# Performance work log

Measured on AMD Instinct MI355X. Metric: run time of the kernel, lower is better.

## Reference

```python
import jax, jax.numpy as jnp
import numpy as np

B, C, H, W = 4, 256, 64, 64
CK = C // 8   # 32, theta/phi channels
CV = C // 2   # 128, g channels


def setup_inputs() -> dict:
    key = jax.random.key(0)
    ks = jax.random.split(key, 10)
    s = lambda fan: 1.0 / np.sqrt(fan)
    inp = {
        "x": jax.random.normal(ks[0], (B, C, H, W), dtype=jnp.float32),
        "theta_w": jax.random.normal(ks[1], (CK, C), dtype=jnp.float32) * s(C),
        "theta_b": jax.random.normal(ks[2], (CK,), dtype=jnp.float32) * 0.01,
        "phi_w": jax.random.normal(ks[3], (CK, C), dtype=jnp.float32) * s(C),
        "phi_b": jax.random.normal(ks[4], (CK,), dtype=jnp.float32) * 0.01,
        "g_w": jax.random.normal(ks[5], (CV, C), dtype=jnp.float32) * s(C),
        "g_b": jax.random.normal(ks[6], (CV,), dtype=jnp.float32) * 0.01,
        "o_w": jax.random.normal(ks[7], (C, CV), dtype=jnp.float32) * s(CV),
        "o_b": jax.random.normal(ks[8], (C,), dtype=jnp.float32) * 0.01,
        "gamma": jax.random.normal(ks[9], (1,), dtype=jnp.float32) * 0.1,
    }
    return inp


def reference(x, theta_w, theta_b, phi_w, phi_b, g_w, g_b, o_w, o_b, gamma):
    b, c, h, w = x.shape
    n = h * w
    xf = x.reshape(b, c, n)  # [B, C, N]
    # 1x1 convs == per-pixel linear projections
    theta = jnp.einsum('oc,bcn->bon', theta_w, xf) + theta_b[None, :, None]  # [B, CK, N]
    phi = jnp.einsum('oc,bcn->bon', phi_w, xf) + phi_b[None, :, None]        # [B, CK, N]
    g = jnp.einsum('oc,bcn->bon', g_w, xf) + g_b[None, :, None]              # [B, CV, N]
    # scores[b, i, j] = theta_i . phi_j ; softmax over dim=1 (query axis i) as in torch code
    scores = jnp.einsum('bci,bcj->bij', theta, phi)  # [B, N, N]
    attention = jax.nn.softmax(scores, axis=1)
    # o_pre = bmm(g, attention^T): o_pre[b, c, i] = sum_j g[b, c, j] * attention[b, i, j]
    o_pre = jnp.einsum('bcj,bij->bci', g, attention)  # [B, CV, N]
    o = jnp.einsum('oc,bcn->bon', o_w, o_pre) + o_b[None, :, None]  # [B, C, N]
    out = (gamma[0] * o + xf).reshape(b, c, h, w)
    return out
```

## Files before the change

kernel.cpp:

```cpp
#include <hip/hip_runtime.h>
#include <math.h>

#define B_  4
#define C_  256
#define N_  4096
#define CK_ 32
#define CV_ 128

typedef __attribute__((ext_vector_type(8))) short short8;
typedef __attribute__((ext_vector_type(4))) float f32x4;
typedef unsigned short u16;
typedef unsigned int   u32;

static constexpr float LOG2E = 1.4426950408889634f;

static __device__ __forceinline__ u16 f2bf(float f) {
    u32 u = __float_as_uint(f);
    u = (u + 0x7FFFu + ((u >> 16) & 1u)) >> 16;
    return (u16)u;
}
static __device__ __forceinline__ float bf2f(u16 h) {
    return __uint_as_float(((u32)h) << 16);
}

__global__ __launch_bounds__(256) void wconv_kernel(
    const float* __restrict__ theta_w, const float* __restrict__ phi_w,
    const float* __restrict__ g_w,     const float* __restrict__ o_w,
    u16* __restrict__ W16, u16* __restrict__ ow16)
{
    const int idx = blockIdx.x * 256 + threadIdx.x;
    if (idx < 8192)        W16[idx] = f2bf(theta_w[idx] * LOG2E);
    else if (idx < 16384)  W16[idx] = f2bf(phi_w[idx - 8192]);
    else if (idx < 49152)  W16[idx] = f2bf(g_w[idx - 16384]);
    else                   ow16[idx - 49152] = f2bf(o_w[idx - 49152]);
}

__global__ __launch_bounds__(256) void xt_kernel(
    const float* __restrict__ x, u16* __restrict__ xT16)
{
    const int b = blockIdx.z, c0 = blockIdx.y * 64, n0 = blockIdx.x * 64;
    const int t = threadIdx.x;
    __shared__ float tile[64][65];

    const int cr = t >> 4, nc = (t & 15) * 4;
    #pragma unroll
    for (int it = 0; it < 4; ++it) {
        const float4 v = *(const float4*)(x + (size_t)(b * C_ + c0 + cr + it * 16) * N_ + n0 + nc);
        tile[cr + it * 16][nc + 0] = v.x; tile[cr + it * 16][nc + 1] = v.y;
        tile[cr + it * 16][nc + 2] = v.z; tile[cr + it * 16][nc + 3] = v.w;
    }
    __syncthreads();
    const int n = t >> 2, cg = (t & 3) * 16;
    union { u16 us[16]; uint4 u4[2]; } pk;
    #pragma unroll
    for (int e = 0; e < 16; ++e) pk.us[e] = f2bf(tile[cg + e][n]);
    uint4* dst = (uint4*)(xT16 + (size_t)(b * N_ + n0 + n) * C_ + c0 + cg);
    dst[0] = pk.u4[0]; dst[1] = pk.u4[1];
}

__global__ __launch_bounds__(256) void proj_mfma_kernel(
    const u16* __restrict__ xT16, const u16* __restrict__ W16,
    const float* __restrict__ theta_b, const float* __restrict__ phi_b,
    const float* __restrict__ g_b,
    u16* __restrict__ theta_t, u16* __restrict__ phi_t, u16* __restrict__ g16)
{
    const int b = blockIdx.y, n0 = blockIdx.x * 64;
    const int w = threadIdx.x >> 6, lane = threadIdx.x & 63;
    const int lr = lane & 15, q = lane >> 4;
    const f32x4 zf = {0.f, 0.f, 0.f, 0.f};

    const u16* xrow = xT16 + (size_t)(b * N_ + n0 + w * 16 + lr) * C_;
    f32x4 acc[4];
    #pragma unroll
    for (int nt = 0; nt < 4; ++nt) acc[nt] = zf;
    for (int ks = 0; ks < 8; ++ks) {
        const short8 aX = *(const short8*)(xrow + ks * 32 + q * 8);
        #pragma unroll
        for (int nt = 0; nt < 4; ++nt) {
            const short8 bW = *(const short8*)(W16 + (size_t)(nt * 16 + lr) * C_ + ks * 32 + q * 8);
            acc[nt] = __builtin_amdgcn_mfma_f32_16x16x32_bf16(aX, bW, acc[nt], 0, 0, 0);
        }
    }
    #pragma unroll
    for (int nt = 0; nt < 4; ++nt) {
        const int o = nt * 16 + lr;
        #pragma unroll
        for (int reg = 0; reg < 4; ++reg) {
            const int n = n0 + w * 16 + q * 4 + reg;
            if (nt < 2)
                theta_t[(size_t)(b * N_ + n) * CK_ + o] = f2bf(acc[nt][reg] + theta_b[o] * LOG2E);
            else
                phi_t[(size_t)(b * N_ + n) * CK_ + (o - 32)] = f2bf(acc[nt][reg] + phi_b[o - 32]);
        }
    }

    #pragma unroll
    for (int mp = 0; mp < 2; ++mp) {
        const int crow = (w * 2 + mp) * 16;
        f32x4 ag[4];
        #pragma unroll
        for (int nt = 0; nt < 4; ++nt) ag[nt] = zf;
        for (int ks = 0; ks < 8; ++ks) {
            const short8 aW = *(const short8*)(W16 + (size_t)(64 + crow + lr) * C_ + ks * 32 + q * 8);
            #pragma unroll
            for (int nt = 0; nt < 4; ++nt) {
                const short8 bX = *(const short8*)(xT16 + (size_t)(b * N_ + n0 + nt * 16 + lr) * C_ + ks * 32 + q * 8);
                ag[nt] = __builtin_amdgcn_mfma_f32_16x16x32_bf16(aW, bX, ag[nt], 0, 0, 0);
            }
        }
        #pragma unroll
        for (int nt = 0; nt < 4; ++nt) {
            #pragma unroll
            for (int reg = 0; reg < 4; ++reg) {
                const int c = crow + q * 4 + reg;
                const int n = n0 + nt * 16 + lr;
                g16[(size_t)(b * CV_ + c) * N_ + n] = f2bf(ag[nt][reg] + g_b[c]);
            }
        }
    }
}

__global__ __launch_bounds__(256) void colstats_kernel(
    const u16* __restrict__ theta_t, const u16* __restrict__ phi_t,
    float* __restrict__ Z)
{
    const int b  = blockIdx.z;
    const int j0 = blockIdx.x * 32;
    const int istart = blockIdx.y * (N_ / 4);
    const int tid = threadIdx.x;
    const int wave = tid >> 6, lane = tid & 63;
    const int lr = lane & 15, q = lane >> 4;

    const int jW = j0 + (wave & 1) * 16;
    const short8 bF = *(const short8*)(phi_t + (size_t)(b * N_ + jW + lr) * CK_ + q * 8);

    const u16* thp = theta_t + (size_t)b * N_ * CK_;
    const f32x4 zero = {0.f, 0.f, 0.f, 0.f};
    float zacc = 0.f;
    for (int it = istart + (wave >> 1) * 16; it < istart + N_ / 4; it += 32) {
        const short8 aF = *(const short8*)(thp + (size_t)(it + lr) * CK_ + q * 8);
        f32x4 S = __builtin_amdgcn_mfma_f32_16x16x32_bf16(aF, bF, zero, 0, 0, 0);
        zacc += exp2f(S[0]) + exp2f(S[1]) + exp2f(S[2]) + exp2f(S[3]);
    }
    zacc += __shfl_xor(zacc, 16);
    zacc += __shfl_xor(zacc, 32);
    if (lane < 16) atomicAdd(&Z[(size_t)b * N_ + jW + lr], zacc);
}

__global__ __launch_bounds__(256) void gscale_kernel(
    u16* __restrict__ g16, const float* __restrict__ Z)
{
    const size_t idx = ((size_t)blockIdx.x * 256 + threadIdx.x) * 8;
    const int n = (int)(idx & (N_ - 1));
    const int b = (int)(idx / ((size_t)CV_ * N_));
    uint4 raw = *(const uint4*)(g16 + idx);
    const float4 z0 = *(const float4*)(Z + (size_t)b * N_ + n);
    const float4 z1 = *(const float4*)(Z + (size_t)b * N_ + n + 4);
    const float zz[8] = {z0.x, z0.y, z0.z, z0.w, z1.x, z1.y, z1.z, z1.w};
    u16* pr = (u16*)&raw;
    union { u16 us[8]; uint4 u4; } pk;
    #pragma unroll
    for (int k = 0; k < 8; ++k) pk.us[k] = f2bf(bf2f(pr[k]) / zz[k]);
    *(uint4*)(g16 + idx) = pk.u4;
}

__global__ __launch_bounds__(512, 4) void opre_kernel(
    const u16* __restrict__ theta_t, const u16* __restrict__ phi_t,
    const u16* __restrict__ g16, float* __restrict__ o_p0, float* __restrict__ o_p1)
{
    const int b = blockIdx.z, jh = blockIdx.y, i0 = blockIdx.x * 64;
    const int w = threadIdx.x >> 6, lane = threadIdx.x & 63;
    const int lr = lane & 15, q = lane >> 4;

    __shared__ u16 El[2][64 * 64];
    __shared__ float rp[16 * 132];

    const int jt = w & 3, it2 = w >> 2;
    const short8 aF0 = *(const short8*)(theta_t + (size_t)(b * N_ + i0 + it2 * 32 + lr) * CK_ + q * 8);
    const short8 aF1 = *(const short8*)(theta_t + (size_t)(b * N_ + i0 + it2 * 32 + 16 + lr) * CK_ + q * 8);

    const int cw = w * 16;
    const u16* gb = g16 + (size_t)(b * CV_ + cw + lr) * N_;
    const u16* pb = phi_t + (size_t)(b * N_) * CK_;

    const f32x4 zf = {0.f, 0.f, 0.f, 0.f};
    f32x4 acc[4];
    #pragma unroll
    for (int nt = 0; nt < 4; ++nt) acc[nt] = zf;

    const int jstart = jh * (N_ / 2), jend = jstart + N_ / 2;
    short8 bF = *(const short8*)(pb + (size_t)(jstart + jt * 16 + lr) * CK_ + q * 8);
    int buf = 0;

    for (int j0 = jstart; j0 < jend; j0 += 64) {
        const short8 gA0 = *(const short8*)(gb + j0 + q * 8);
        const short8 gA1 = *(const short8*)(gb + j0 + 32 + q * 8);

        const f32x4 S0 = __builtin_amdgcn_mfma_f32_16x16x32_bf16(aF0, bF, zf, 0, 0, 0);
        const f32x4 S1 = __builtin_amdgcn_mfma_f32_16x16x32_bf16(aF1, bF, zf, 0, 0, 0);

        const int jn = (j0 + 64 < jend) ? j0 + 64 : jstart;
        bF = *(const short8*)(pb + (size_t)(jn + jt * 16 + lr) * CK_ + q * 8);

        u16* Eb = El[buf];
        const int jcol = jt * 16 + lr;
        #pragma unroll
        for (int reg = 0; reg < 4; ++reg) {
            const int ia = it2 * 32 + q * 4 + reg;
            Eb[ia * 64 + ((((jcol >> 3) ^ (ia & 7)) << 3) | (jcol & 7))] = f2bf(exp2f(S0[reg]));
            const int ib = ia + 16;
            Eb[ib * 64 + ((((jcol >> 3) ^ (ib & 7)) << 3) | (jcol & 7))] = f2bf(exp2f(S1[reg]));
        }
        __syncthreads();

        #pragma unroll
        for (int nt = 0; nt < 4; ++nt) {
            const int row = nt * 16 + lr;
            const short8 bE0 = *(const short8*)(Eb + row * 64 + ((q ^ (row & 7)) << 3));
            const short8 bE1 = *(const short8*)(Eb + row * 64 + (((4 + q) ^ (row & 7)) << 3));
            acc[nt] = __builtin_amdgcn_mfma_f32_16x16x32_bf16(gA0, bE0, acc[nt], 0, 0, 0);
            acc[nt] = __builtin_amdgcn_mfma_f32_16x16x32_bf16(gA1, bE1, acc[nt], 0, 0, 0);
        }
        buf ^= 1;
    }

    __syncthreads();
    float* op = (jh ? o_p1 : o_p0) + (size_t)(b * N_ + i0) * CV_;
    #pragma unroll
    for (int p = 0; p < 4; ++p) {
        #pragma unroll
        for (int reg = 0; reg < 4; ++reg)
            rp[lr * 132 + cw + q * 4 + reg] = acc[p][reg];
        __syncthreads();
        const int t = threadIdx.x;
        const int ir = t >> 5, cc = (t & 31) * 4;
        *(float4*)(op + (size_t)(p * 16 + ir) * CV_ + cc) = *(const float4*)(rp + ir * 132 + cc);
        __syncthreads();
    }
}

__global__ __launch_bounds__(256) void final_mfma_kernel(
    const float* __restrict__ o_p0, const float* __restrict__ o_p1,
    const u16* __restrict__ ow16, const float* __restrict__ o_b,
    const float* __restrict__ gamma, const float* __restrict__ x,
    float* __restrict__ out)
{
    const int b = blockIdx.y, n0 = blockIdx.x * 64;
    const int w = threadIdx.x >> 6, lane = threadIdx.x & 63;
    const int lr = lane & 15, q = lane >> 4;
    const f32x4 zf = {0.f, 0.f, 0.f, 0.f};

    f32x4 acc[4][4];
    #pragma unroll
    for (int mt = 0; mt < 4; ++mt)
        #pragma unroll
        for (int nt = 0; nt < 4; ++nt) acc[mt][nt] = zf;

    const float* p0 = o_p0 + (size_t)(b * N_ + n0) * CV_;
    const float* p1 = o_p1 + (size_t)(b * N_ + n0) * CV_;

    for (int ks = 0; ks < 4; ++ks) {
        short8 bP[4];
        #pragma unroll
        for (int nt = 0; nt < 4; ++nt) {
            const size_t base = (size_t)(nt * 16 + lr) * CV_ + ks * 32 + q * 8;
            const float4 a0 = *(const float4*)(p0 + base);
            const float4 a1 = *(const float4*)(p0 + base + 4);
            const float4 b0 = *(const float4*)(p1 + base);
            const float4 b1 = *(const float4*)(p1 + base + 4);
            union { u16 us[8]; short8 s8; } pk;
            pk.us[0] = f2bf(a0.x + b0.x); pk.us[1] = f2bf(a0.y + b0.y);
            pk.us[2] = f2bf(a0.z + b0.z); pk.us[3] = f2bf(a0.w + b0.w);
            pk.us[4] = f2bf(a1.x + b1.x); pk.us[5] = f2bf(a1.y + b1.y);
            pk.us[6] = f2bf(a1.z + b1.z); pk.us[7] = f2bf(a1.w + b1.w);
            bP[nt] = pk.s8;
        }
        #pragma unroll
        for (int mt = 0; mt < 4; ++mt) {
            const short8 aW = *(const short8*)(ow16 + (size_t)((w * 4 + mt) * 16 + lr) * CV_ + ks * 32 + q * 8);
            #pragma unroll
            for (int nt = 0; nt < 4; ++nt)
                acc[mt][nt] = __builtin_amdgcn_mfma_f32_16x16x32_bf16(aW, bP[nt], acc[mt][nt], 0, 0, 0);
        }
    }

    const float gm = gamma[0];
    #pragma unroll
    for (int mt = 0; mt < 4; ++mt) {
        #pragma unroll
        for (int nt = 0; nt < 4; ++nt) {
            #pragma unroll
            for (int reg = 0; reg < 4; ++reg) {
                const int oc = (w * 4 + mt) * 16 + q * 4 + reg;
                const int n = n0 + nt * 16 + lr;
                const size_t off = (size_t)(b * C_ + oc) * N_ + n;
                out[off] = x[off] + gm * (acc[mt][nt][reg] + o_b[oc]);
            }
        }
    }
}

extern "C" void kernel_launch(void* const* d_in, const int* in_sizes, int n_in,
                              void* d_out, int out_size, void* d_ws, size_t ws_size,
                              hipStream_t stream)
{
    const float* x       = (const float*)d_in[0];
    const float* theta_w = (const float*)d_in[1];
    const float* theta_b = (const float*)d_in[2];
    const float* phi_w   = (const float*)d_in[3];
    const float* phi_b   = (const float*)d_in[4];
    const float* g_w     = (const float*)d_in[5];
    const float* g_b     = (const float*)d_in[6];
    const float* o_w     = (const float*)d_in[7];
    const float* o_b     = (const float*)d_in[8];
    const float* gamma   = (const float*)d_in[9];
    float* out = (float*)d_out;

    u16* xT16    = (u16*)d_ws;
    u16* W16     = xT16 + (size_t)B_ * N_ * C_;
    u16* ow16    = W16 + 192 * C_;
    u16* theta_t = ow16 + C_ * CV_;
    u16* phi_t   = theta_t + (size_t)B_ * N_ * CK_;
    u16* g16     = phi_t + (size_t)B_ * N_ * CK_;
    float* Z     = (float*)(g16 + (size_t)B_ * CV_ * N_);
    float* o_p0  = Z + (size_t)B_ * N_;
    float* o_p1  = o_p0 + (size_t)B_ * N_ * CV_;

    hipMemsetAsync(Z, 0, (size_t)B_ * N_ * sizeof(float), stream);

    wconv_kernel<<<dim3(320), 256, 0, stream>>>(theta_w, phi_w, g_w, o_w, W16, ow16);
    xt_kernel<<<dim3(N_ / 64, C_ / 64, B_), 256, 0, stream>>>(x, xT16);
    proj_mfma_kernel<<<dim3(N_ / 64, B_), 256, 0, stream>>>(
        xT16, W16, theta_b, phi_b, g_b, theta_t, phi_t, g16);
    colstats_kernel<<<dim3(N_ / 32, 4, B_), 256, 0, stream>>>(theta_t, phi_t, Z);
    gscale_kernel<<<dim3((B_ * CV_ * N_) / 2048), 256, 0, stream>>>(g16, Z);
    opre_kernel<<<dim3(N_ / 64, 2, B_), 512, 0, stream>>>(theta_t, phi_t, g16, o_p0, o_p1);
    final_mfma_kernel<<<dim3(N_ / 64, B_), 256, 0, stream>>>(
        o_p0, o_p1, ow16, o_b, gamma, x, out);
}
```

Baseline: 205.4 us.

## Fold softmax normalization into opre, keep E in registers, bf16 partials

Drops the gscale pass and applies the reciprocal column sums inside opre. opre now computes S transposed (phi as A, theta as B), so the exp results already sit in the MFMA A-operand layout for the 16x16x16 bf16 MFMA with g. This removes the LDS round-trip and the per-tile __syncthreads. The j axis is split four ways instead of two, partial outputs are stored as bf16 instead of fp32, and the final kernel sums four bf16 partials. proj and final also gain an extra grid dimension for more parallelism. The risks are added bf16 rounding in the partial sums and more reads in final, and the mfma16 fallback silently returns the accumulator when the 16x16x16 builtin is missing.

```diff
diff --git a/kernel.cpp b/kernel.cpp
--- a/kernel.cpp
+++ b/kernel.cpp
@@ -8,6 +8,7 @@
 #define CV_ 128
 
 typedef __attribute__((ext_vector_type(8))) short short8;
+typedef __attribute__((ext_vector_type(4))) short short4v;
 typedef __attribute__((ext_vector_type(4))) float f32x4;
 typedef unsigned short u16;
 typedef unsigned int   u32;
@@ -21,6 +22,19 @@
 }
 static __device__ __forceinline__ float bf2f(u16 h) {
     return __uint_as_float(((u32)h) << 16);
+}
+static __device__ __forceinline__ u32 pack2bf(float a, float b) {
+    const u32 ua = (__float_as_uint(a) + 0x8000u) >> 16;
+    const u32 ub = (__float_as_uint(b) + 0x8000u) & 0xFFFF0000u;
+    return ua | ub;
+}
+
+static __device__ __forceinline__ f32x4 mfma16(short4v a, short4v b, f32x4 c) {
+#if __has_builtin(__builtin_amdgcn_mfma_f32_16x16x16bf16_1k)
+    return __builtin_amdgcn_mfma_f32_16x16x16bf16_1k(a, b, c, 0, 0, 0);
+#else
+    return c;
+#endif
 }
 
 __global__ __launch_bounds__(256) void wconv_kernel(
@@ -64,39 +78,38 @@
     const float* __restrict__ g_b,
     u16* __restrict__ theta_t, u16* __restrict__ phi_t, u16* __restrict__ g16)
 {
-    const int b = blockIdx.y, n0 = blockIdx.x * 64;
+    const int b = blockIdx.z, n0 = blockIdx.x * 64, phase = blockIdx.y;
     const int w = threadIdx.x >> 6, lane = threadIdx.x & 63;
     const int lr = lane & 15, q = lane >> 4;
     const f32x4 zf = {0.f, 0.f, 0.f, 0.f};
 
-    const u16* xrow = xT16 + (size_t)(b * N_ + n0 + w * 16 + lr) * C_;
-    f32x4 acc[4];
-    #pragma unroll
-    for (int nt = 0; nt < 4; ++nt) acc[nt] = zf;
-    for (int ks = 0; ks < 8; ++ks) {
-        const short8 aX = *(const short8*)(xrow + ks * 32 + q * 8);
+    if (phase == 0) {
+        const u16* xrow = xT16 + (size_t)(b * N_ + n0 + w * 16 + lr) * C_;
+        f32x4 acc[4];
+        #pragma unroll
+        for (int nt = 0; nt < 4; ++nt) acc[nt] = zf;
+        for (int ks = 0; ks < 8; ++ks) {
+            const short8 aX = *(const short8*)(xrow + ks * 32 + q * 8);
+            #pragma unroll
+            for (int nt = 0; nt < 4; ++nt) {
+                const short8 bW = *(const short8*)(W16 + (size_t)(nt * 16 + lr) * C_ + ks * 32 + q * 8);
+                acc[nt] = __builtin_amdgcn_mfma_f32_16x16x32_bf16(aX, bW, acc[nt], 0, 0, 0);
+            }
+        }
         #pragma unroll
         for (int nt = 0; nt < 4; ++nt) {
-            const short8 bW = *(const short8*)(W16 + (size_t)(nt * 16 + lr) * C_ + ks * 32 + q * 8);
-            acc[nt] = __builtin_amdgcn_mfma_f32_16x16x32_bf16(aX, bW, acc[nt], 0, 0, 0);
-        }
-    }
-    #pragma unroll
-    for (int nt = 0; nt < 4; ++nt) {
-        const int o = nt * 16 + lr;
-        #pragma unroll
-        for (int reg = 0; reg < 4; ++reg) {
-            const int n = n0 + w * 16 + q * 4 + reg;
-            if (nt < 2)
-                theta_t[(size_t)(b * N_ + n) * CK_ + o] = f2bf(acc[nt][reg] + theta_b[o] * LOG2E);
-            else
-                phi_t[(size_t)(b * N_ + n) * CK_ + (o - 32)] = f2bf(acc[nt][reg] + phi_b[o - 32]);
-        }
-    }
-
-    #pragma unroll
-    for (int mp = 0; mp < 2; ++mp) {
-        const int crow = (w * 2 + mp) * 16;
+            const int o = nt * 16 + lr;
+            #pragma unroll
+            for (int reg = 0; reg < 4; ++reg) {
+                const int n = n0 + w * 16 + q * 4 + reg;
+                if (nt < 2)
+                    theta_t[(size_t)(b * N_ + n) * CK_ + o] = f2bf(acc[nt][reg] + theta_b[o] * LOG2E);
+                else
+                    phi_t[(size_t)(b * N_ + n) * CK_ + (o - 32)] = f2bf(acc[nt][reg] + phi_b[o - 32]);
+            }
+        }
+    } else {
+        const int crow = (phase - 1) * 64 + w * 16;
         f32x4 ag[4];
         #pragma unroll
         for (int nt = 0; nt < 4; ++nt) ag[nt] = zf;
@@ -147,137 +160,133 @@
     if (lane < 16) atomicAdd(&Z[(size_t)b * N_ + jW + lr], zacc);
 }
 
-__global__ __launch_bounds__(256) void gscale_kernel(
-    u16* __restrict__ g16, const float* __restrict__ Z)
-{
-    const size_t idx = ((size_t)blockIdx.x * 256 + threadIdx.x) * 8;
-    const int n = (int)(idx & (N_ - 1));
-    const int b = (int)(idx / ((size_t)CV_ * N_));
-    uint4 raw = *(const uint4*)(g16 + idx);
-    const float4 z0 = *(const float4*)(Z + (size_t)b * N_ + n);
-    const float4 z1 = *(const float4*)(Z + (size_t)b * N_ + n + 4);
-    const float zz[8] = {z0.x, z0.y, z0.z, z0.w, z1.x, z1.y, z1.z, z1.w};
-    u16* pr = (u16*)&raw;
-    union { u16 us[8]; uint4 u4; } pk;
-    #pragma unroll
-    for (int k = 0; k < 8; ++k) pk.us[k] = f2bf(bf2f(pr[k]) / zz[k]);
-    *(uint4*)(g16 + idx) = pk.u4;
-}
-
-__global__ __launch_bounds__(512, 4) void opre_kernel(
+__global__ __launch_bounds__(256, 2) void opre_kernel(
     const u16* __restrict__ theta_t, const u16* __restrict__ phi_t,
-    const u16* __restrict__ g16, float* __restrict__ o_p0, float* __restrict__ o_p1)
-{
-    const int b = blockIdx.z, jh = blockIdx.y, i0 = blockIdx.x * 64;
+    const u16* __restrict__ g16, const float* __restrict__ Z,
+    u16* __restrict__ o_p)
+{
+    const int b = blockIdx.z, jh = blockIdx.y;
     const int w = threadIdx.x >> 6, lane = threadIdx.x & 63;
     const int lr = lane & 15, q = lane >> 4;
-
-    __shared__ u16 El[2][64 * 64];
-    __shared__ float rp[16 * 132];
-
-    const int jt = w & 3, it2 = w >> 2;
-    const short8 aF0 = *(const short8*)(theta_t + (size_t)(b * N_ + i0 + it2 * 32 + lr) * CK_ + q * 8);
-    const short8 aF1 = *(const short8*)(theta_t + (size_t)(b * N_ + i0 + it2 * 32 + 16 + lr) * CK_ + q * 8);
-
-    const int cw = w * 16;
-    const u16* gb = g16 + (size_t)(b * CV_ + cw + lr) * N_;
+    const int i0 = blockIdx.x * 128 + w * 32;
+
+    __shared__ u16 ep[4][32 * 136];
+
+    short8 thB[2];
+    #pragma unroll
+    for (int it = 0; it < 2; ++it)
+        thB[it] = *(const short8*)(theta_t + (size_t)(b * N_ + i0 + it * 16 + lr) * CK_ + q * 8);
+
+    f32x4 acc[2][8];
+    #pragma unroll
+    for (int it = 0; it < 2; ++it)
+        #pragma unroll
+        for (int ct = 0; ct < 8; ++ct) acc[it][ct] = (f32x4){0.f, 0.f, 0.f, 0.f};
+
+    const f32x4 zf = {0.f, 0.f, 0.f, 0.f};
     const u16* pb = phi_t + (size_t)(b * N_) * CK_;
-
-    const f32x4 zf = {0.f, 0.f, 0.f, 0.f};
-    f32x4 acc[4];
-    #pragma unroll
-    for (int nt = 0; nt < 4; ++nt) acc[nt] = zf;
-
-    const int jstart = jh * (N_ / 2), jend = jstart + N_ / 2;
-    short8 bF = *(const short8*)(pb + (size_t)(jstart + jt * 16 + lr) * CK_ + q * 8);
-    int buf = 0;
-
-    for (int j0 = jstart; j0 < jend; j0 += 64) {
-        const short8 gA0 = *(const short8*)(gb + j0 + q * 8);
-        const short8 gA1 = *(const short8*)(gb + j0 + 32 + q * 8);
-
-        const f32x4 S0 = __builtin_amdgcn_mfma_f32_16x16x32_bf16(aF0, bF, zf, 0, 0, 0);
-        const f32x4 S1 = __builtin_amdgcn_mfma_f32_16x16x32_bf16(aF1, bF, zf, 0, 0, 0);
-
-        const int jn = (j0 + 64 < jend) ? j0 + 64 : jstart;
-        bF = *(const short8*)(pb + (size_t)(jn + jt * 16 + lr) * CK_ + q * 8);
-
-        u16* Eb = El[buf];
-        const int jcol = jt * 16 + lr;
-        #pragma unroll
-        for (int reg = 0; reg < 4; ++reg) {
-            const int ia = it2 * 32 + q * 4 + reg;
-            Eb[ia * 64 + ((((jcol >> 3) ^ (ia & 7)) << 3) | (jcol & 7))] = f2bf(exp2f(S0[reg]));
-            const int ib = ia + 16;
-            Eb[ib * 64 + ((((jcol >> 3) ^ (ib & 7)) << 3) | (jcol & 7))] = f2bf(exp2f(S1[reg]));
-        }
-        __syncthreads();
-
-        #pragma unroll
-        for (int nt = 0; nt < 4; ++nt) {
-            const int row = nt * 16 + lr;
-            const short8 bE0 = *(const short8*)(Eb + row * 64 + ((q ^ (row & 7)) << 3));
-            const short8 bE1 = *(const short8*)(Eb + row * 64 + (((4 + q) ^ (row & 7)) << 3));
-            acc[nt] = __builtin_amdgcn_mfma_f32_16x16x32_bf16(gA0, bE0, acc[nt], 0, 0, 0);
-            acc[nt] = __builtin_amdgcn_mfma_f32_16x16x32_bf16(gA1, bE1, acc[nt], 0, 0, 0);
-        }
-        buf ^= 1;
-    }
-
-    __syncthreads();
-    float* op = (jh ? o_p1 : o_p0) + (size_t)(b * N_ + i0) * CV_;
-    #pragma unroll
-    for (int p = 0; p < 4; ++p) {
-        #pragma unroll
-        for (int reg = 0; reg < 4; ++reg)
-            rp[lr * 132 + cw + q * 4 + reg] = acc[p][reg];
-        __syncthreads();
-        const int t = threadIdx.x;
-        const int ir = t >> 5, cc = (t & 31) * 4;
-        *(float4*)(op + (size_t)(p * 16 + ir) * CV_ + cc) = *(const float4*)(rp + ir * 132 + cc);
-        __syncthreads();
+    const float* Zb = Z + (size_t)b * N_;
+    const int jstart = jh * (N_ / 4);
+
+    for (int j0 = jstart; j0 < jstart + N_ / 4; j0 += 64) {
+        short8 phA[4];
+        float4 zv[4];
+        #pragma unroll
+        for (int jt = 0; jt < 4; ++jt) {
+            phA[jt] = *(const short8*)(pb + (size_t)(j0 + jt * 16 + lr) * CK_ + q * 8);
+            zv[jt]  = *(const float4*)(Zb + j0 + jt * 16 + q * 4);
+        }
+
+        short4v a2[2][4];
+        #pragma unroll
+        for (int jt = 0; jt < 4; ++jt) {
+            const float rz0 = __builtin_amdgcn_rcpf(zv[jt].x);
+            const float rz1 = __builtin_amdgcn_rcpf(zv[jt].y);
+            const float rz2 = __builtin_amdgcn_rcpf(zv[jt].z);
+            const float rz3 = __builtin_amdgcn_rcpf(zv[jt].w);
+            #pragma unroll
+            for (int it = 0; it < 2; ++it) {
+                const f32x4 S = __builtin_amdgcn_mfma_f32_16x16x32_bf16(phA[jt], thB[it], zf, 0, 0, 0);
+                const float e0 = exp2f(S[0]) * rz0;
+                const float e1 = exp2f(S[1]) * rz1;
+                const float e2 = exp2f(S[2]) * rz2;
+                const float e3 = exp2f(S[3]) * rz3;
+                union { u32 u[2]; short4v s; } pk;
+                pk.u[0] = pack2bf(e0, e1);
+                pk.u[1] = pack2bf(e2, e3);
+                a2[it][jt] = pk.s;
+            }
+        }
+
+        #pragma unroll
+        for (int ct = 0; ct < 8; ++ct) {
+            const u16* gp = g16 + (size_t)(b * CV_ + ct * 16 + lr) * N_ + j0 + q * 4;
+            #pragma unroll
+            for (int jt = 0; jt < 4; ++jt) {
+                const short4v gB = *(const short4v*)(gp + jt * 16);
+                acc[0][ct] = mfma16(a2[0][jt], gB, acc[0][ct]);
+                acc[1][ct] = mfma16(a2[1][jt], gB, acc[1][ct]);
+            }
+        }
+    }
+
+    u16* myep = ep[w];
+    #pragma unroll
+    for (int it = 0; it < 2; ++it)
+        #pragma unroll
+        for (int ct = 0; ct < 8; ++ct)
+            #pragma unroll
+            for (int reg = 0; reg < 4; ++reg)
+                myep[(it * 16 + q * 4 + reg) * 136 + ct * 16 + lr] = f2bf(acc[it][ct][reg]);
+    __builtin_amdgcn_s_waitcnt(0);
+
+    u16* op = o_p + ((size_t)(jh * B_ + b) * N_) * CV_;
+    #pragma unroll
+    for (int inst = 0; inst < 8; ++inst) {
+        const int row = inst * 4 + q;
+        const uint4 v = *(const uint4*)(myep + row * 136 + lr * 8);
+        *(uint4*)(op + (size_t)(i0 + row) * CV_ + lr * 8) = v;
     }
 }
 
 __global__ __launch_bounds__(256) void final_mfma_kernel(
-    const float* __restrict__ o_p0, const float* __restrict__ o_p1,
-    const u16* __restrict__ ow16, const float* __restrict__ o_b,
-    const float* __restrict__ gamma, const float* __restrict__ x,
-    float* __restrict__ out)
-{
-    const int b = blockIdx.y, n0 = blockIdx.x * 64;
+    const u16* __restrict__ o_p, const u16* __restrict__ ow16,
+    const float* __restrict__ o_b, const float* __restrict__ gamma,
+    const float* __restrict__ x, float* __restrict__ out)
+{
+    const int b = blockIdx.z, ych = blockIdx.y, n0 = blockIdx.x * 64;
     const int w = threadIdx.x >> 6, lane = threadIdx.x & 63;
     const int lr = lane & 15, q = lane >> 4;
-    const f32x4 zf = {0.f, 0.f, 0.f, 0.f};
-
-    f32x4 acc[4][4];
-    #pragma unroll
-    for (int mt = 0; mt < 4; ++mt)
-        #pragma unroll
-        for (int nt = 0; nt < 4; ++nt) acc[mt][nt] = zf;
-
-    const float* p0 = o_p0 + (size_t)(b * N_ + n0) * CV_;
-    const float* p1 = o_p1 + (size_t)(b * N_ + n0) * CV_;
+    const size_t PSTRIDE = (size_t)B_ * N_ * CV_;
+
+    f32x4 acc[2][4];
+    #pragma unroll
+    for (int mt = 0; mt < 2; ++mt)
+        #pragma unroll
+        for (int nt = 0; nt < 4; ++nt) acc[mt][nt] = (f32x4){0.f, 0.f, 0.f, 0.f};
 
     for (int ks = 0; ks < 4; ++ks) {
         short8 bP[4];
         #pragma unroll
         for (int nt = 0; nt < 4; ++nt) {
-            const size_t base = (size_t)(nt * 16 + lr) * CV_ + ks * 32 + q * 8;
-            const float4 a0 = *(const float4*)(p0 + base);
-            const float4 a1 = *(const float4*)(p0 + base + 4);
-            const float4 b0 = *(const float4*)(p1 + base);
-            const float4 b1 = *(const float4*)(p1 + base + 4);
+            const size_t pbase = (size_t)(b * N_ + n0 + nt * 16 + lr) * CV_ + ks * 32 + q * 8;
+            float s[8] = {0.f, 0.f, 0.f, 0.f, 0.f, 0.f, 0.f, 0.f};
+            #pragma unroll
+            for (int part = 0; part < 4; ++part) {
+                const uint4 raw = *(const uint4*)(o_p + part * PSTRIDE + pbase);
+                const u16* pr = (const u16*)&raw;
+                #pragma unroll
+                for (int e = 0; e < 8; ++e) s[e] += bf2f(pr[e]);
+            }
             union { u16 us[8]; short8 s8; } pk;
-            pk.us[0] = f2bf(a0.x + b0.x); pk.us[1] = f2bf(a0.y + b0.y);
-            pk.us[2] = f2bf(a0.z + b0.z); pk.us[3] = f2bf(a0.w + b0.w);
-            pk.us[4] = f2bf(a1.x + b1.x); pk.us[5] = f2bf(a1.y + b1.y);
-            pk.us[6] = f2bf(a1.z + b1.z); pk.us[7] = f2bf(a1.w + b1.w);
+            #pragma unroll
+            for (int e = 0; e < 8; ++e) pk.us[e] = f2bf(s[e]);
             bP[nt] = pk.s8;
         }
         #pragma unroll
-        for (int mt = 0; mt < 4; ++mt) {
-            const short8 aW = *(const short8*)(ow16 + (size_t)((w * 4 + mt) * 16 + lr) * CV_ + ks * 32 + q * 8);
+        for (int mt = 0; mt < 2; ++mt) {
+            const int ocb = ych * 128 + (w * 2 + mt) * 16;
+            const short8 aW = *(const short8*)(ow16 + (size_t)(ocb + lr) * CV_ + ks * 32 + q * 8);
             #pragma unroll
             for (int nt = 0; nt < 4; ++nt)
                 acc[mt][nt] = __builtin_amdgcn_mfma_f32_16x16x32_bf16(aW, bP[nt], acc[mt][nt], 0, 0, 0);
@@ -286,12 +295,12 @@
 
     const float gm = gamma[0];
     #pragma unroll
-    for (int mt = 0; mt < 4; ++mt) {
+    for (int mt = 0; mt < 2; ++mt) {
         #pragma unroll
         for (int nt = 0; nt < 4; ++nt) {
             #pragma unroll
             for (int reg = 0; reg < 4; ++reg) {
-                const int oc = (w * 4 + mt) * 16 + q * 4 + reg;
+                const int oc = ych * 128 + (w * 2 + mt) * 16 + q * 4 + reg;
                 const int n = n0 + nt * 16 + lr;
                 const size_t off = (size_t)(b * C_ + oc) * N_ + n;
                 out[off] = x[off] + gm * (acc[mt][nt][reg] + o_b[oc]);
@@ -323,18 +332,16 @@
     u16* phi_t   = theta_t + (size_t)B_ * N_ * CK_;
     u16* g16     = phi_t + (size_t)B_ * N_ * CK_;
     float* Z     = (float*)(g16 + (size_t)B_ * CV_ * N_);
-    float* o_p0  = Z + (size_t)B_ * N_;
-    float* o_p1  = o_p0 + (size_t)B_ * N_ * CV_;
-
-    hipMemsetAsync(Z, 0, (size_t)B_ * N_ * sizeof(float), stream);
+    u16* o_p     = (u16*)(Z + (size_t)B_ * N_);
+
+    (void)hipMemsetAsync(Z, 0, (size_t)B_ * N_ * sizeof(float), stream);
 
     wconv_kernel<<<dim3(320), 256, 0, stream>>>(theta_w, phi_w, g_w, o_w, W16, ow16);
     xt_kernel<<<dim3(N_ / 64, C_ / 64, B_), 256, 0, stream>>>(x, xT16);
-    proj_mfma_kernel<<<dim3(N_ / 64, B_), 256, 0, stream>>>(
+    proj_mfma_kernel<<<dim3(N_ / 64, 3, B_), 256, 0, stream>>>(
         xT16, W16, theta_b, phi_b, g_b, theta_t, phi_t, g16);
     colstats_kernel<<<dim3(N_ / 32, 4, B_), 256, 0, stream>>>(theta_t, phi_t, Z);
-    gscale_kernel<<<dim3((B_ * CV_ * N_) / 2048), 256, 0, stream>>>(g16, Z);
-    opre_kernel<<<dim3(N_ / 64, 2, B_), 512, 0, stream>>>(theta_t, phi_t, g16, o_p0, o_p1);
-    final_mfma_kernel<<<dim3(N_ / 64, B_), 256, 0, stream>>>(
-        o_p0, o_p1, ow16, o_b, gamma, x, out);
-}
+    opre_kernel<<<dim3(N_ / 128, 4, B_), 256, 0, stream>>>(theta_t, phi_t, g16, Z, o_p);
+    final_mfma_kernel<<<dim3(N_ / 64, 2, B_), 256, 0, stream>>>(
+        o_p, ow16, o_b, gamma, x, out);
+}
```

Measured after the change: 282.6 us. 1.38x slower.

## Split projection and output kernels across more blocks, store bf16 partials

Applied to the files above, without the earlier changes.

The projection kernel is split into three phases over a new grid dimension: theta/phi in one phase and two halves of g in the others. This gives three times as many blocks. In the attention kernel each warp now computes a 2x2 tile of 32 channels by 32 queries instead of 16 channels by 64 queries. Partial outputs are written directly as bf16, which drops the shared-memory staging and halves partial-buffer traffic. The final kernel is split four ways over output channels so more blocks run with fewer accumulators. The cost is an extra bf16 rounding of the partial sums, and the attention tiles now reload g from global memory per k-step.

```diff
diff --git a/kernel.cpp b/kernel.cpp
--- a/kernel.cpp
+++ b/kernel.cpp
@@ -64,39 +64,38 @@
     const float* __restrict__ g_b,
     u16* __restrict__ theta_t, u16* __restrict__ phi_t, u16* __restrict__ g16)
 {
-    const int b = blockIdx.y, n0 = blockIdx.x * 64;
+    const int b = blockIdx.z, n0 = blockIdx.x * 64, phase = blockIdx.y;
     const int w = threadIdx.x >> 6, lane = threadIdx.x & 63;
     const int lr = lane & 15, q = lane >> 4;
     const f32x4 zf = {0.f, 0.f, 0.f, 0.f};
 
-    const u16* xrow = xT16 + (size_t)(b * N_ + n0 + w * 16 + lr) * C_;
-    f32x4 acc[4];
-    #pragma unroll
-    for (int nt = 0; nt < 4; ++nt) acc[nt] = zf;
-    for (int ks = 0; ks < 8; ++ks) {
-        const short8 aX = *(const short8*)(xrow + ks * 32 + q * 8);
+    if (phase == 0) {
+        const u16* xrow = xT16 + (size_t)(b * N_ + n0 + w * 16 + lr) * C_;
+        f32x4 acc[4];
+        #pragma unroll
+        for (int nt = 0; nt < 4; ++nt) acc[nt] = zf;
+        for (int ks = 0; ks < 8; ++ks) {
+            const short8 aX = *(const short8*)(xrow + ks * 32 + q * 8);
+            #pragma unroll
+            for (int nt = 0; nt < 4; ++nt) {
+                const short8 bW = *(const short8*)(W16 + (size_t)(nt * 16 + lr) * C_ + ks * 32 + q * 8);
+                acc[nt] = __builtin_amdgcn_mfma_f32_16x16x32_bf16(aX, bW, acc[nt], 0, 0, 0);
+            }
+        }
         #pragma unroll
         for (int nt = 0; nt < 4; ++nt) {
-            const short8 bW = *(const short8*)(W16 + (size_t)(nt * 16 + lr) * C_ + ks * 32 + q * 8);
-            acc[nt] = __builtin_amdgcn_mfma_f32_16x16x32_bf16(aX, bW, acc[nt], 0, 0, 0);
-        }
-    }
-    #pragma unroll
-    for (int nt = 0; nt < 4; ++nt) {
-        const int o = nt * 16 + lr;
-        #pragma unroll
-        for (int reg = 0; reg < 4; ++reg) {
-            const int n = n0 + w * 16 + q * 4 + reg;
-            if (nt < 2)
-                theta_t[(size_t)(b * N_ + n) * CK_ + o] = f2bf(acc[nt][reg] + theta_b[o] * LOG2E);
-            else
-                phi_t[(size_t)(b * N_ + n) * CK_ + (o - 32)] = f2bf(acc[nt][reg] + phi_b[o - 32]);
-        }
-    }
-
-    #pragma unroll
-    for (int mp = 0; mp < 2; ++mp) {
-        const int crow = (w * 2 + mp) * 16;
+            const int o = nt * 16 + lr;
+            #pragma unroll
+            for (int reg = 0; reg < 4; ++reg) {
+                const int n = n0 + w * 16 + q * 4 + reg;
+                if (nt < 2)
+                    theta_t[(size_t)(b * N_ + n) * CK_ + o] = f2bf(acc[nt][reg] + theta_b[o] * LOG2E);
+                else
+                    phi_t[(size_t)(b * N_ + n) * CK_ + (o - 32)] = f2bf(acc[nt][reg] + phi_b[o - 32]);
+            }
+        }
+    } else {
+        const int crow = (phase - 1) * 64 + w * 16;
         f32x4 ag[4];
         #pragma unroll
         for (int nt = 0; nt < 4; ++nt) ag[nt] = zf;
@@ -164,38 +163,36 @@
     *(uint4*)(g16 + idx) = pk.u4;
 }
 
-__global__ __launch_bounds__(512, 4) void opre_kernel(
+__global__ __launch_bounds__(512) void opre_kernel(
     const u16* __restrict__ theta_t, const u16* __restrict__ phi_t,
-    const u16* __restrict__ g16, float* __restrict__ o_p0, float* __restrict__ o_p1)
+    const u16* __restrict__ g16, u16* __restrict__ o_p)
 {
     const int b = blockIdx.z, jh = blockIdx.y, i0 = blockIdx.x * 64;
     const int w = threadIdx.x >> 6, lane = threadIdx.x & 63;
     const int lr = lane & 15, q = lane >> 4;
 
     __shared__ u16 El[2][64 * 64];
-    __shared__ float rp[16 * 132];
 
     const int jt = w & 3, it2 = w >> 2;
     const short8 aF0 = *(const short8*)(theta_t + (size_t)(b * N_ + i0 + it2 * 32 + lr) * CK_ + q * 8);
     const short8 aF1 = *(const short8*)(theta_t + (size_t)(b * N_ + i0 + it2 * 32 + 16 + lr) * CK_ + q * 8);
 
-    const int cw = w * 16;
-    const u16* gb = g16 + (size_t)(b * CV_ + cw + lr) * N_;
+    const int cg = w & 3, ig = w >> 2;
+    const u16* gb = g16 + (size_t)(b * CV_ + cg * 32) * N_;
+
+    f32x4 acc[2][2];
+    #pragma unroll
+    for (int mt = 0; mt < 2; ++mt)
+        #pragma unroll
+        for (int nt = 0; nt < 2; ++nt) acc[mt][nt] = (f32x4){0.f, 0.f, 0.f, 0.f};
+
+    const f32x4 zf = {0.f, 0.f, 0.f, 0.f};
     const u16* pb = phi_t + (size_t)(b * N_) * CK_;
-
-    const f32x4 zf = {0.f, 0.f, 0.f, 0.f};
-    f32x4 acc[4];
-    #pragma unroll
-    for (int nt = 0; nt < 4; ++nt) acc[nt] = zf;
-
     const int jstart = jh * (N_ / 2), jend = jstart + N_ / 2;
     short8 bF = *(const short8*)(pb + (size_t)(jstart + jt * 16 + lr) * CK_ + q * 8);
     int buf = 0;
 
     for (int j0 = jstart; j0 < jend; j0 += 64) {
-        const short8 gA0 = *(const short8*)(gb + j0 + q * 8);
-        const short8 gA1 = *(const short8*)(gb + j0 + 32 + q * 8);
-
         const f32x4 S0 = __builtin_amdgcn_mfma_f32_16x16x32_bf16(aF0, bF, zf, 0, 0, 0);
         const f32x4 S1 = __builtin_amdgcn_mfma_f32_16x16x32_bf16(aF1, bF, zf, 0, 0, 0);
 
@@ -214,88 +211,77 @@
         __syncthreads();
 
         #pragma unroll
-        for (int nt = 0; nt < 4; ++nt) {
-            const int row = nt * 16 + lr;
-            const short8 bE0 = *(const short8*)(Eb + row * 64 + ((q ^ (row & 7)) << 3));
-            const short8 bE1 = *(const short8*)(Eb + row * 64 + (((4 + q) ^ (row & 7)) << 3));
-            acc[nt] = __builtin_amdgcn_mfma_f32_16x16x32_bf16(gA0, bE0, acc[nt], 0, 0, 0);
-            acc[nt] = __builtin_amdgcn_mfma_f32_16x16x32_bf16(gA1, bE1, acc[nt], 0, 0, 0);
+        for (int ks = 0; ks < 2; ++ks) {
+            short8 bE[2];
+            #pragma unroll
+            for (int nt = 0; nt < 2; ++nt) {
+                const int row = ig * 32 + nt * 16 + lr;
+                bE[nt] = *(const short8*)(Eb + row * 64 + (((ks * 4 + q) ^ (row & 7)) << 3));
+            }
+            #pragma unroll
+            for (int mt = 0; mt < 2; ++mt) {
+                const short8 gA = *(const short8*)(gb + (size_t)(mt * 16 + lr) * N_ + j0 + ks * 32 + q * 8);
+                acc[mt][0] = __builtin_amdgcn_mfma_f32_16x16x32_bf16(gA, bE[0], acc[mt][0], 0, 0, 0);
+                acc[mt][1] = __builtin_amdgcn_mfma_f32_16x16x32_bf16(gA, bE[1], acc[mt][1], 0, 0, 0);
+            }
         }
         buf ^= 1;
     }
 
-    __syncthreads();
-    float* op = (jh ? o_p1 : o_p0) + (size_t)(b * N_ + i0) * CV_;
-    #pragma unroll
-    for (int p = 0; p < 4; ++p) {
-        #pragma unroll
-        for (int reg = 0; reg < 4; ++reg)
-            rp[lr * 132 + cw + q * 4 + reg] = acc[p][reg];
-        __syncthreads();
-        const int t = threadIdx.x;
-        const int ir = t >> 5, cc = (t & 31) * 4;
-        *(float4*)(op + (size_t)(p * 16 + ir) * CV_ + cc) = *(const float4*)(rp + ir * 132 + cc);
-        __syncthreads();
+    u16* op = o_p + (size_t)(jh * B_ + b) * N_ * CV_;
+    #pragma unroll
+    for (int mt = 0; mt < 2; ++mt) {
+        #pragma unroll
+        for (int nt = 0; nt < 2; ++nt) {
+            union { u16 us[4]; uint2 u2; } pk;
+            #pragma unroll
+            for (int reg = 0; reg < 4; ++reg) pk.us[reg] = f2bf(acc[mt][nt][reg]);
+            *(uint2*)(op + (size_t)(i0 + ig * 32 + nt * 16 + lr) * CV_ + cg * 32 + mt * 16 + q * 4) = pk.u2;
+        }
     }
 }
 
 __global__ __launch_bounds__(256) void final_mfma_kernel(
-    const float* __restrict__ o_p0, const float* __restrict__ o_p1,
-    const u16* __restrict__ ow16, const float* __restrict__ o_b,
-    const float* __restrict__ gamma, const float* __restrict__ x,
-    float* __restrict__ out)
-{
-    const int b = blockIdx.y, n0 = blockIdx.x * 64;
+    const u16* __restrict__ o_p, const u16* __restrict__ ow16,
+    const float* __restrict__ o_b, const float* __restrict__ gamma,
+    const float* __restrict__ x, float* __restrict__ out)
+{
+    const int b = blockIdx.z, ych = blockIdx.y, n0 = blockIdx.x * 64;
     const int w = threadIdx.x >> 6, lane = threadIdx.x & 63;
     const int lr = lane & 15, q = lane >> 4;
-    const f32x4 zf = {0.f, 0.f, 0.f, 0.f};
-
-    f32x4 acc[4][4];
-    #pragma unroll
-    for (int mt = 0; mt < 4; ++mt)
-        #pragma unroll
-        for (int nt = 0; nt < 4; ++nt) acc[mt][nt] = zf;
-
-    const float* p0 = o_p0 + (size_t)(b * N_ + n0) * CV_;
-    const float* p1 = o_p1 + (size_t)(b * N_ + n0) * CV_;
+    const size_t PSTRIDE = (size_t)B_ * N_ * CV_;
+
+    f32x4 acc[4];
+    #pragma unroll
+    for (int nt = 0; nt < 4; ++nt) acc[nt] = (f32x4){0.f, 0.f, 0.f, 0.f};
+
+    const int ocb = ych * 64 + w * 16;
 
     for (int ks = 0; ks < 4; ++ks) {
-        short8 bP[4];
+        const short8 aW = *(const short8*)(ow16 + (size_t)(ocb + lr) * CV_ + ks * 32 + q * 8);
         #pragma unroll
         for (int nt = 0; nt < 4; ++nt) {
-            const size_t base = (size_t)(nt * 16 + lr) * CV_ + ks * 32 + q * 8;
-            const float4 a0 = *(const float4*)(p0 + base);
-            const float4 a1 = *(const float4*)(p0 + base + 4);
-            const float4 b0 = *(const float4*)(p1 + base);
-            const float4 b1 = *(const float4*)(p1 + base + 4);
+            const size_t pbase = (size_t)(b * N_ + n0 + nt * 16 + lr) * CV_ + ks * 32 + q * 8;
+            const uint4 r0 = *(const uint4*)(o_p + pbase);
+            const uint4 r1 = *(const uint4*)(o_p + PSTRIDE + pbase);
+            const u16* p0 = (const u16*)&r0;
+            const u16* p1 = (const u16*)&r1;
             union { u16 us[8]; short8 s8; } pk;
-            pk.us[0] = f2bf(a0.x + b0.x); pk.us[1] = f2bf(a0.y + b0.y);
-            pk.us[2] = f2bf(a0.z + b0.z); pk.us[3] = f2bf(a0.w + b0.w);
-            pk.us[4] = f2bf(a1.x + b1.x); pk.us[5] = f2bf(a1.y + b1.y);
-            pk.us[6] = f2bf(a1.z + b1.z); pk.us[7] = f2bf(a1.w + b1.w);
-            bP[nt] = pk.s8;
-        }
-        #pragma unroll
-        for (int mt = 0; mt < 4; ++mt) {
-            const short8 aW = *(const short8*)(ow16 + (size_t)((w * 4 + mt) * 16 + lr) * CV_ + ks * 32 + q * 8);
-            #pragma unroll
-            for (int nt = 0; nt < 4; ++nt)
-                acc[mt][nt] = __builtin_amdgcn_mfma_f32_16x16x32_bf16(aW, bP[nt], acc[mt][nt], 0, 0, 0);
+            #pragma unroll
+            for (int e = 0; e < 8; ++e) pk.us[e] = f2bf(bf2f(p0[e]) + bf2f(p1[e]));
+            acc[nt] = __builtin_amdgcn_mfma_f32_16x16x32_bf16(aW, pk.s8, acc[nt], 0, 0, 0);
         }
     }
 
     const float gm = gamma[0];
     #pragma unroll
-    for (int mt = 0; mt < 4; ++mt) {
-        #pragma unroll
-        for (int nt = 0; nt < 4; ++nt) {
-            #pragma unroll
-            for (int reg = 0; reg < 4; ++reg) {
-                const int oc = (w * 4 + mt) * 16 + q * 4 + reg;
-                const int n = n0 + nt * 16 + lr;
-                const size_t off = (size_t)(b * C_ + oc) * N_ + n;
-                out[off] = x[off] + gm * (acc[mt][nt][reg] + o_b[oc]);
-            }
+    for (int nt = 0; nt < 4; ++nt) {
+        #pragma unroll
+        for (int reg = 0; reg < 4; ++reg) {
+            const int oc = ocb + q * 4 + reg;
+            const int n = n0 + nt * 16 + lr;
+            const size_t off = (size_t)(b * C_ + oc) * N_ + n;
+            out[off] = x[off] + gm * (acc[nt][reg] + o_b[oc]);
         }
     }
 }
@@ -323,18 +309,17 @@
     u16* phi_t   = theta_t + (size_t)B_ * N_ * CK_;
     u16* g16     = phi_t + (size_t)B_ * N_ * CK_;
     float* Z     = (float*)(g16 + (size_t)B_ * CV_ * N_);
-    float* o_p0  = Z + (size_t)B_ * N_;
-    float* o_p1  = o_p0 + (size_t)B_ * N_ * CV_;
-
-    hipMemsetAsync(Z, 0, (size_t)B_ * N_ * sizeof(float), stream);
+    u16* o_p     = (u16*)(Z + (size_t)B_ * N_);
+
+    (void)hipMemsetAsync(Z, 0, (size_t)B_ * N_ * sizeof(float), stream);
 
     wconv_kernel<<<dim3(320), 256, 0, stream>>>(theta_w, phi_w, g_w, o_w, W16, ow16);
     xt_kernel<<<dim3(N_ / 64, C_ / 64, B_), 256, 0, stream>>>(x, xT16);
-    proj_mfma_kernel<<<dim3(N_ / 64, B_), 256, 0, stream>>>(
+    proj_mfma_kernel<<<dim3(N_ / 64, 3, B_), 256, 0, stream>>>(
         xT16, W16, theta_b, phi_b, g_b, theta_t, phi_t, g16);
     colstats_kernel<<<dim3(N_ / 32, 4, B_), 256, 0, stream>>>(theta_t, phi_t, Z);
     gscale_kernel<<<dim3((B_ * CV_ * N_) / 2048), 256, 0, stream>>>(g16, Z);
-    opre_kernel<<<dim3(N_ / 64, 2, B_), 512, 0, stream>>>(theta_t, phi_t, g16, o_p0, o_p1);
-    final_mfma_kernel<<<dim3(N_ / 64, B_), 256, 0, stream>>>(
-        o_p0, o_p1, ow16, o_b, gamma, x, out);
-}
+    opre_kernel<<<dim3(N_ / 64, 2, B_), 512, 0, stream>>>(theta_t, phi_t, g16, o_p);
+    final_mfma_kernel<<<dim3(N_ / 64, 4, B_), 256, 0, stream>>>(
+        o_p, ow16, o_b, gamma, x, out);
+}
```

New measurement: 219.7 us. +7.0%, slower.
